# Optimization experiments

Measured on AMD Instinct MI355X. Metric: run time of the kernel, lower is better.

Reference implementation:

```python
import jax, jax.numpy as jnp
import numpy as np

BLOCK_SIZE = 16


def _rope(x, positions):
    # Faithful to PrecomputedRotaryEmbedding: neg_mask = [-1,1] tiled, rotate halves.
    # x: [B, H, D], positions: [B] int (the module uses positions = context_lens)
    B, H, D = x.shape
    inv_freq = 1.0 / (10000.0 ** (jnp.arange(0, D, 2, dtype=jnp.float32) / D))  # [D/2]
    freqs = positions.astype(jnp.float32)[:, None] * inv_freq                    # [B, D/2]
    emb = jnp.concatenate([freqs, freqs], axis=-1)                               # [B, D]
    cos = jnp.cos(emb)[:, None, :]
    sin = jnp.sin(emb)[:, None, :]
    neg_mask = jnp.tile(jnp.array([-1.0, 1.0], dtype=x.dtype), D // 2)           # [D]
    xr = x * neg_mask
    xr = jnp.concatenate([xr[..., D // 2:], xr[..., :D // 2]], axis=-1)
    return x * cos + xr * sin


def setup_inputs() -> dict:
    k0 = jax.random.key(0)
    ks = jax.random.split(k0, 6)
    B, H, Hkv, D = 32, 32, 8, 128
    max_blocks, bs = 128, BLOCK_SIZE
    num_blocks = B * max_blocks  # 4096
    query = jax.random.normal(ks[0], (B, H, D), dtype=jnp.float32)
    key = jax.random.normal(ks[1], (B, Hkv, D), dtype=jnp.float32)
    value = jax.random.normal(ks[2], (B, Hkv, D), dtype=jnp.float32)
    k_cache = jax.random.normal(ks[3], (num_blocks, bs, Hkv, D), dtype=jnp.float32)
    v_cache = jax.random.normal(ks[4], (num_blocks, bs, Hkv, D), dtype=jnp.float32)
    block_table = jnp.arange(B * max_blocks, dtype=jnp.int32).reshape(B, max_blocks)
    context_lens = jax.random.randint(ks[5], (B,), 1, 2048).astype(jnp.int32)
    return {"query": query, "key": key, "value": value, "k_cache": k_cache,
            "v_cache": v_cache, "block_table": block_table, "context_lens": context_lens}


def reference(query, key, value, k_cache, v_cache, block_table, context_lens):
    B, H, D = query.shape
    Hkv = key.shape[1]
    num_blocks, bs, _, _ = k_cache.shape
    max_blocks = block_table.shape[1]
    L = max_blocks * bs
    scale = D ** -0.5

    # 1) RoPE on q and new k (module uses positions = context_lens)
    q = _rope(query, context_lens)
    k_new = _rope(key, context_lens)

    # 2) scatter new k/v into paged cache at slot of token (ctx-1)
    tok = context_lens - 1
    slots = block_table[jnp.arange(B), tok // bs] * bs + tok % bs                # [B]
    kf = k_cache.reshape(num_blocks * bs, Hkv, D).at[slots].set(k_new)
    vf = v_cache.reshape(num_blocks * bs, Hkv, D).at[slots].set(value)

    # 3) block-table gather: per-seq contiguous KV view [B, L, Hkv, D]
    tok_idx = (block_table[:, :, None] * bs
               + jnp.arange(bs, dtype=jnp.int32)[None, None, :]).reshape(B, L)
    kg = kf[tok_idx]
    vg = vf[tok_idx]

    # 4) single-token GQA attention over first context_lens[b] tokens
    G = H // Hkv
    qg = q.reshape(B, Hkv, G, D)
    scores = jnp.einsum('bgrd,blgd->bgrl', qg, kg) * scale                       # [B,Hkv,G,L]
    valid = jnp.arange(L, dtype=jnp.int32)[None, :] < context_lens[:, None]      # [B,L]
    scores = jnp.where(valid[:, None, None, :], scores, -jnp.inf)
    attn = jax.nn.softmax(scores, axis=-1)
    out = jnp.einsum('bgrl,blgd->bgrd', attn, vg).reshape(B, H, D)
    return out
```

## Files before the change

### kernel.cpp

```cpp
#include <hip/hip_runtime.h>
#include <math.h>

#define NB   32
#define NH   32
#define HKV  8
#define GQ   4
#define DD   128
#define BS   16
#define MAXBLK 128
#define LMAX 2048
#define CHUNK 256
#define NCHUNK (LMAX / CHUNK)

typedef float fx4 __attribute__((ext_vector_type(4)));

__global__ __launch_bounds__(256) void rope_prep(
    const float* __restrict__ q, const float* __restrict__ k,
    const int* __restrict__ ctx, float* __restrict__ qrope,
    float* __restrict__ krope)
{
    int b = blockIdx.x;
    float pos = (float)ctx[b];
    const float QSCALE = 0.08838834764831845f;
    for (int i = threadIdx.x; i < (NH + HKV) * DD; i += blockDim.x) {
        int row = i >> 7;
        int d   = i & (DD - 1);
        int j   = d & 63;
        float ang = pos * __expf(-(float)j * 0.14391156831212787f);
        float sv, cv;
        sincosf(ang, &sv, &cv);
        float sign = (d & 1) ? 1.0f : -1.0f;
        if (row < NH) {
            const float* src = q + ((size_t)b * NH + row) * DD;
            float v = src[d] * cv + sign * src[d ^ 64] * sv;
            qrope[((size_t)b * NH + row) * DD + d] = v * QSCALE;
        } else {
            int kvh = row - NH;
            const float* src = k + ((size_t)b * HKV + kvh) * DD;
            float v = src[d] * cv + sign * src[d ^ 64] * sv;
            krope[((size_t)b * HKV + kvh) * DD + d] = v;
        }
    }
}

__global__ __launch_bounds__(256) void attn_partial(
    const float* __restrict__ kcache, const float* __restrict__ vcache,
    const float* __restrict__ qrope,  const float* __restrict__ krope,
    const float* __restrict__ vnew,   const int* __restrict__ btab,
    const int* __restrict__ ctx,      float* __restrict__ pacc,
    float* __restrict__ pml)
{
    int c   = blockIdx.x;
    int kvh = blockIdx.y;
    int b   = blockIdx.z;
    int L   = ctx[b];
    int start = c * CHUNK;
    if (start >= L) return;
    int end = min(start + CHUNK, L);

    __shared__ int   s_bt[CHUNK / BS];
    __shared__ float s_q[GQ][DD];
    __shared__ float s_acc[8][GQ][DD];
    __shared__ float s_m[8];
    __shared__ float s_l[8][GQ];

    int tid = threadIdx.x;
    if (tid < CHUNK / BS)
        s_bt[tid] = btab[b * MAXBLK + c * (CHUNK / BS) + tid];
    for (int i = tid; i < GQ * DD; i += 256)
        ((float*)s_q)[i] = qrope[(size_t)(b * NH + kvh * GQ) * DD + i];
    __syncthreads();

    int w    = tid >> 6;
    int lane = tid & 63;
    int half = lane >> 5;
    int lq   = lane & 31;

    fx4 qf[GQ];
    #pragma unroll
    for (int g = 0; g < GQ; g++) qf[g] = *(const fx4*)&s_q[g][lq * 4];

    float m = -INFINITY;
    float lsum[GQ] = {0.f, 0.f, 0.f, 0.f};
    fx4   acc[GQ];
    #pragma unroll
    for (int g = 0; g < GQ; g++) acc[g] = (fx4)(0.f);

    const fx4* knew  = (const fx4*)&krope[(size_t)(b * HKV + kvh) * DD];
    const fx4* vnewr = (const fx4*)&vnew [(size_t)(b * HKV + kvh) * DD];

    int t = start + w * 2 + half;
    if (t < end) {
        int blk = s_bt[(t - start) >> 4];
        size_t base = ((size_t)(blk * BS + (t & (BS - 1))) * HKV + kvh) * DD;
        bool nw = (t == L - 1);
        fx4 kf = nw ? knew[lq]
                    : __builtin_nontemporal_load(((const fx4*)&kcache[base]) + lq);
        fx4 vf = nw ? vnewr[lq]
                    : __builtin_nontemporal_load(((const fx4*)&vcache[base]) + lq);

        while (true) {
            int tn = t + 8;
            fx4 kf2, vf2;
            if (tn < end) {
                int blk2 = s_bt[(tn - start) >> 4];
                size_t base2 = ((size_t)(blk2 * BS + (tn & (BS - 1))) * HKV + kvh) * DD;
                bool nw2 = (tn == L - 1);
                kf2 = nw2 ? knew[lq]
                          : __builtin_nontemporal_load(((const fx4*)&kcache[base2]) + lq);
                vf2 = nw2 ? vnewr[lq]
                          : __builtin_nontemporal_load(((const fx4*)&vcache[base2]) + lq);
            }
            float sg[GQ];
            #pragma unroll
            for (int g = 0; g < GQ; g++)
                sg[g] = qf[g].x * kf.x + qf[g].y * kf.y
                      + qf[g].z * kf.z + qf[g].w * kf.w;
            #pragma unroll
            for (int off = 1; off < 32; off <<= 1) {
                #pragma unroll
                for (int g = 0; g < GQ; g++)
                    sg[g] += __shfl_xor(sg[g], off, 64);
            }
            float smax = fmaxf(fmaxf(sg[0], sg[1]), fmaxf(sg[2], sg[3]));
            if (smax > m) {
                float corr = __expf(m - smax);
                #pragma unroll
                for (int g = 0; g < GQ; g++) {
                    lsum[g] *= corr;
                    acc[g] *= corr;
                }
                m = smax;
            }
            #pragma unroll
            for (int g = 0; g < GQ; g++) {
                float p = __expf(sg[g] - m);
                lsum[g] += p;
                acc[g] += p * vf;
            }
            if (tn >= end) break;
            t = tn; kf = kf2; vf = vf2;
        }
    }

    int stream = w * 2 + half;
    #pragma unroll
    for (int g = 0; g < GQ; g++)
        *(fx4*)&s_acc[stream][g][lq * 4] = acc[g];
    if (lq == 0) {
        s_m[stream] = m;
        #pragma unroll
        for (int g = 0; g < GQ; g++) s_l[stream][g] = lsum[g];
    }
    __syncthreads();

    float M = s_m[0];
    #pragma unroll
    for (int s = 1; s < 8; s++) M = fmaxf(M, s_m[s]);
    float f[8];
    #pragma unroll
    for (int s = 0; s < 8; s++) f[s] = __expf(s_m[s] - M);

    size_t pbase = (size_t)(b * HKV + kvh) * NCHUNK + c;
    for (int idx = tid; idx < GQ * DD; idx += 256) {
        int g = idx >> 7;
        int d = idx & (DD - 1);
        float A = 0.f;
        #pragma unroll
        for (int s = 0; s < 8; s++) A += s_acc[s][g][d] * f[s];
        pacc[pbase * (GQ * DD) + idx] = A;
        if (d == 0) {
            float Lg = 0.f;
            #pragma unroll
            for (int s = 0; s < 8; s++) Lg += s_l[s][g] * f[s];
            pml[pbase * 8 + g] = Lg;
        }
    }
    if (tid == 0) pml[pbase * 8 + 4] = M;
}

__global__ __launch_bounds__(256) void attn_reduce(
    const float* __restrict__ pacc, const float* __restrict__ pml,
    const int* __restrict__ ctx, float* __restrict__ out)
{
    int bk  = blockIdx.x;
    int b   = bk >> 3;
    int kvh = bk & 7;
    int L   = ctx[b];
    int nc  = (L + CHUNK - 1) / CHUNK;
    const float* ml = &pml[(size_t)bk * NCHUNK * 8];

    float M = -INFINITY;
    for (int cc = 0; cc < nc; cc++) M = fmaxf(M, ml[cc * 8 + 4]);

    float fct[NCHUNK];
    for (int cc = 0; cc < nc; cc++) fct[cc] = __expf(ml[cc * 8 + 4] - M);

    for (int idx = threadIdx.x; idx < GQ * DD; idx += 256) {
        int g = idx >> 7;
        int d = idx & (DD - 1);
        float A = 0.f, Lg = 0.f;
        for (int cc = 0; cc < nc; cc++) {
            A  += pacc[((size_t)bk * NCHUNK + cc) * (GQ * DD) + idx] * fct[cc];
            Lg += ml[cc * 8 + g] * fct[cc];
        }
        out[((size_t)b * NH + kvh * GQ + g) * DD + d] = A / Lg;
    }
}

extern "C" void kernel_launch(void* const* d_in, const int* in_sizes, int n_in,
                              void* d_out, int out_size, void* d_ws, size_t ws_size,
                              hipStream_t stream)
{
    const float* q   = (const float*)d_in[0];
    const float* k   = (const float*)d_in[1];
    const float* v   = (const float*)d_in[2];
    const float* kc  = (const float*)d_in[3];
    const float* vc  = (const float*)d_in[4];
    const int*   bt  = (const int*)d_in[5];
    const int*   ctx = (const int*)d_in[6];
    float*       out = (float*)d_out;

    float* ws    = (float*)d_ws;
    float* qrope = ws;
    float* krope = qrope + (size_t)NB * NH * DD;
    float* pacc  = krope + (size_t)NB * HKV * DD;
    float* pml   = pacc + (size_t)NB * HKV * NCHUNK * GQ * DD;

    rope_prep<<<NB, 256, 0, stream>>>(q, k, ctx, qrope, krope);
    attn_partial<<<dim3(NCHUNK, HKV, NB), 256, 0, stream>>>(
        kc, vc, qrope, krope, v, bt, ctx, pacc, pml);
    attn_reduce<<<NB * HKV, 256, 0, stream>>>(pacc, pml, ctx, out);
}
```

Before: 514.2 us.

## Fuse RoPE into attention kernel and deepen KV prefetch to two steps

Removes the separate rope_prep launch and computes RoPE for the four query heads and the new key directly inside each attention block, keeping them in shared memory. This saves a kernel launch and a round trip through global memory, at the cost of recomputing the rotation in every chunk block. The KV loop also changes from one-ahead to two-ahead register prefetch, putting more loads in flight per thread but using more registers.

```diff
diff --git a/kernel.cpp b/kernel.cpp
--- a/kernel.cpp
+++ b/kernel.cpp
@@ -14,38 +14,9 @@
 
 typedef float fx4 __attribute__((ext_vector_type(4)));
 
-__global__ __launch_bounds__(256) void rope_prep(
-    const float* __restrict__ q, const float* __restrict__ k,
-    const int* __restrict__ ctx, float* __restrict__ qrope,
-    float* __restrict__ krope)
-{
-    int b = blockIdx.x;
-    float pos = (float)ctx[b];
-    const float QSCALE = 0.08838834764831845f;
-    for (int i = threadIdx.x; i < (NH + HKV) * DD; i += blockDim.x) {
-        int row = i >> 7;
-        int d   = i & (DD - 1);
-        int j   = d & 63;
-        float ang = pos * __expf(-(float)j * 0.14391156831212787f);
-        float sv, cv;
-        sincosf(ang, &sv, &cv);
-        float sign = (d & 1) ? 1.0f : -1.0f;
-        if (row < NH) {
-            const float* src = q + ((size_t)b * NH + row) * DD;
-            float v = src[d] * cv + sign * src[d ^ 64] * sv;
-            qrope[((size_t)b * NH + row) * DD + d] = v * QSCALE;
-        } else {
-            int kvh = row - NH;
-            const float* src = k + ((size_t)b * HKV + kvh) * DD;
-            float v = src[d] * cv + sign * src[d ^ 64] * sv;
-            krope[((size_t)b * HKV + kvh) * DD + d] = v;
-        }
-    }
-}
-
 __global__ __launch_bounds__(256) void attn_partial(
     const float* __restrict__ kcache, const float* __restrict__ vcache,
-    const float* __restrict__ qrope,  const float* __restrict__ krope,
+    const float* __restrict__ qin,    const float* __restrict__ kin,
     const float* __restrict__ vnew,   const int* __restrict__ btab,
     const int* __restrict__ ctx,      float* __restrict__ pacc,
     float* __restrict__ pml)
@@ -60,6 +31,7 @@
 
     __shared__ int   s_bt[CHUNK / BS];
     __shared__ float s_q[GQ][DD];
+    __shared__ float s_k[DD];
     __shared__ float s_acc[8][GQ][DD];
     __shared__ float s_m[8];
     __shared__ float s_l[8][GQ];
@@ -67,14 +39,34 @@
     int tid = threadIdx.x;
     if (tid < CHUNK / BS)
         s_bt[tid] = btab[b * MAXBLK + c * (CHUNK / BS) + tid];
-    for (int i = tid; i < GQ * DD; i += 256)
-        ((float*)s_q)[i] = qrope[(size_t)(b * NH + kvh * GQ) * DD + i];
+
+    {
+        float pos = (float)L;
+        const float QSCALE = 0.08838834764831845f;
+        for (int i = tid; i < (GQ + 1) * DD; i += 256) {
+            int row = i >> 7;
+            int d   = i & (DD - 1);
+            int j   = d & 63;
+            float ang = pos * __expf(-(float)j * 0.14391156831212787f);
+            float sv, cv;
+            sincosf(ang, &sv, &cv);
+            float sign = (d & 1) ? 1.0f : -1.0f;
+            if (row < GQ) {
+                const float* src = qin + ((size_t)(b * NH + kvh * GQ + row)) * DD;
+                s_q[row][d] = (src[d] * cv + sign * src[d ^ 64] * sv) * QSCALE;
+            } else {
+                const float* src = kin + ((size_t)(b * HKV + kvh)) * DD;
+                s_k[d] = src[d] * cv + sign * src[d ^ 64] * sv;
+            }
+        }
+    }
     __syncthreads();
 
     int w    = tid >> 6;
     int lane = tid & 63;
     int half = lane >> 5;
     int lq   = lane & 31;
+    int stream = w * 2 + half;
 
     fx4 qf[GQ];
     #pragma unroll
@@ -86,36 +78,36 @@
     #pragma unroll
     for (int g = 0; g < GQ; g++) acc[g] = (fx4)(0.f);
 
-    const fx4* knew  = (const fx4*)&krope[(size_t)(b * HKV + kvh) * DD];
-    const fx4* vnewr = (const fx4*)&vnew [(size_t)(b * HKV + kvh) * DD];
-
-    int t = start + w * 2 + half;
-    if (t < end) {
+    const fx4* vnewr = (const fx4*)&vnew[(size_t)(b * HKV + kvh) * DD];
+
+    auto load_kv = [&](int t, fx4& kf, fx4& vf) {
         int blk = s_bt[(t - start) >> 4];
         size_t base = ((size_t)(blk * BS + (t & (BS - 1))) * HKV + kvh) * DD;
-        bool nw = (t == L - 1);
-        fx4 kf = nw ? knew[lq]
-                    : __builtin_nontemporal_load(((const fx4*)&kcache[base]) + lq);
-        fx4 vf = nw ? vnewr[lq]
-                    : __builtin_nontemporal_load(((const fx4*)&vcache[base]) + lq);
-
+        if (t == L - 1) {
+            kf = *(const fx4*)&s_k[lq * 4];
+            vf = vnewr[lq];
+        } else {
+            kf = __builtin_nontemporal_load(((const fx4*)&kcache[base]) + lq);
+            vf = __builtin_nontemporal_load(((const fx4*)&vcache[base]) + lq);
+        }
+    };
+
+    int t = start + stream;
+    if (t < end) {
+        fx4 kfA, vfA, kfB, vfB;
+        load_kv(t, kfA, vfA);
+        bool has1 = (t + 8) < end;
+        if (has1) load_kv(t + 8, kfB, vfB);
         while (true) {
-            int tn = t + 8;
-            fx4 kf2, vf2;
-            if (tn < end) {
-                int blk2 = s_bt[(tn - start) >> 4];
-                size_t base2 = ((size_t)(blk2 * BS + (tn & (BS - 1))) * HKV + kvh) * DD;
-                bool nw2 = (tn == L - 1);
-                kf2 = nw2 ? knew[lq]
-                          : __builtin_nontemporal_load(((const fx4*)&kcache[base2]) + lq);
-                vf2 = nw2 ? vnewr[lq]
-                          : __builtin_nontemporal_load(((const fx4*)&vcache[base2]) + lq);
-            }
+            int t2 = t + 16;
+            bool has2 = t2 < end;
+            fx4 kfC, vfC;
+            if (has2) load_kv(t2, kfC, vfC);
             float sg[GQ];
             #pragma unroll
             for (int g = 0; g < GQ; g++)
-                sg[g] = qf[g].x * kf.x + qf[g].y * kf.y
-                      + qf[g].z * kf.z + qf[g].w * kf.w;
+                sg[g] = qf[g].x * kfA.x + qf[g].y * kfA.y
+                      + qf[g].z * kfA.z + qf[g].w * kfA.w;
             #pragma unroll
             for (int off = 1; off < 32; off <<= 1) {
                 #pragma unroll
@@ -136,14 +128,15 @@
             for (int g = 0; g < GQ; g++) {
                 float p = __expf(sg[g] - m);
                 lsum[g] += p;
-                acc[g] += p * vf;
-            }
-            if (tn >= end) break;
-            t = tn; kf = kf2; vf = vf2;
-        }
-    }
-
-    int stream = w * 2 + half;
+                acc[g] += p * vfA;
+            }
+            if (!has1) break;
+            kfA = kfB; vfA = vfB; kfB = kfC; vfB = vfC;
+            has1 = has2;
+            t += 8;
+        }
+    }
+
     #pragma unroll
     for (int g = 0; g < GQ; g++)
         *(fx4*)&s_acc[stream][g][lq * 4] = acc[g];
@@ -221,14 +214,11 @@
     const int*   ctx = (const int*)d_in[6];
     float*       out = (float*)d_out;
 
-    float* ws    = (float*)d_ws;
-    float* qrope = ws;
-    float* krope = qrope + (size_t)NB * NH * DD;
-    float* pacc  = krope + (size_t)NB * HKV * DD;
-    float* pml   = pacc + (size_t)NB * HKV * NCHUNK * GQ * DD;
-
-    rope_prep<<<NB, 256, 0, stream>>>(q, k, ctx, qrope, krope);
+    float* ws   = (float*)d_ws;
+    float* pacc = ws;
+    float* pml  = pacc + (size_t)NB * HKV * NCHUNK * GQ * DD;
+
     attn_partial<<<dim3(NCHUNK, HKV, NB), 256, 0, stream>>>(
-        kc, vc, qrope, krope, v, bt, ctx, pacc, pml);
+        kc, vc, q, k, v, bt, ctx, pacc, pml);
     attn_reduce<<<NB * HKV, 256, 0, stream>>>(pacc, pml, ctx, out);
 }
```

Result: faster. 490.7 us (-4.6%).
